# Kernel optimization log

Hardware: AMD Instinct MI355X
Metric: run time of the kernel (lower is better)

## Reference

```python
import jax, jax.numpy as jnp
import numpy as np

MAX_LENGTH = 400
NULL_TERM_IND = 52
THR = 1.0 - 1e-05  # F.threshold threshold value


def leaky(x):
    # F.leaky_relu default negative_slope=0.01
    return jnp.where(x >= 0, x, 0.01 * x)


def gru_cell(x, h, w_ih, w_hh, b_ih, b_hh):
    # torch.nn.GRUCell math
    gi = x @ w_ih.T + b_ih          # [B, 3H]
    gh = h @ w_hh.T + b_hh          # [B, 3H]
    i_r, i_z, i_n = jnp.split(gi, 3, axis=-1)
    h_r, h_z, h_n = jnp.split(gh, 3, axis=-1)
    r = jax.nn.sigmoid(i_r + h_r)
    z = jax.nn.sigmoid(i_z + h_z)
    n = jnp.tanh(i_n + r * h_n)
    return (1.0 - z) * n + z * h


def setup_inputs() -> dict:
    key = jax.random.key(0)
    ks = jax.random.split(key, 9)
    B, D, H, C = 2048, 4096, 128, 96
    def init(k, shape, fan):
        return (jax.random.uniform(k, shape, jnp.float32) * 2.0 - 1.0) / np.sqrt(fan)
    return {
        "img_feat": jax.random.normal(ks[0], (B, D), jnp.float32),
        "lin1_w": init(ks[1], (H, D), D),
        "lin1_b": init(ks[2], (H,), D),
        "w_ih": init(ks[3], (3 * H, H), H),
        "w_hh": init(ks[4], (3 * H, H), H),
        "b_ih": init(ks[5], (3 * H,), H),
        "b_hh": init(ks[6], (3 * H,), H),
        "lin2_w": init(ks[7], (C, H), H),
        "lin2_b": init(ks[8], (C,), H),
    }


def reference(img_feat, lin1_w, lin1_b, w_ih, w_hh, b_ih, b_hh, lin2_w, lin2_b):
    # ht: GRU input at t=0 is leaky_relu(lin1(img_feat)); hidden starts at zeros.
    ht = leaky(img_feat @ lin1_w.T + lin1_b)   # [B, 128]
    h0 = jnp.zeros_like(ht)

    def step(carry, _):
        ht, h0 = carry
        hn = gru_cell(ht, h0, w_ih, w_hh, b_ih, b_hh)
        # original: ht = char_gen(ht, h0); h0 = ht -> input == hidden next step
        chars = leaky(hn) @ lin2_w.T + lin2_b   # [B, C]
        m = jax.lax.stop_gradient(jnp.max(chars, axis=-1, keepdims=True))  # .data detach
        cn = chars / m
        cn = jnp.where(cn > THR, cn, 0.0)       # F.threshold(x, 1-1e-5, 0)
        return (hn, hn), cn

    _, titles = jax.lax.scan(step, (ht, h0), None, length=MAX_LENGTH)  # [T, B, C]
    titles = jnp.transpose(titles, (1, 0, 2))   # [B, T, C]

    # title_lens: first t with titles[b, t, NULL_TERM_IND] == 1, else MAX_LENGTH
    eq = titles[:, :, NULL_TERM_IND] == 1.0     # [B, T]
    first = jnp.argmax(eq, axis=1)
    lens = jnp.where(eq.any(axis=1), first + 1, MAX_LENGTH).astype(jnp.int32)
    return titles, lens
```

## Files before the change

kernel.cpp:

```cpp
#include <hip/hip_runtime.h>
#include <math.h>

#define NB   8
#define TT   400
#define HH   128
#define CC   96
#define DD   4096
#define THRV (1.0f - 1e-5f)
#define XR   40
#define HEPS 4e-6f
#define CHP  128
#define S10  1024.0f
#define IS10 0.0009765625f
#define IS20 9.5367431640625e-07f

typedef _Float16 f16x8 __attribute__((ext_vector_type(8)));
typedef float    f32x4 __attribute__((ext_vector_type(4)));

__device__ __forceinline__ float rcp_fast(float x) {
#if __has_builtin(__builtin_amdgcn_rcpf)
    return __builtin_amdgcn_rcpf(x);
#else
    return 1.0f / x;
#endif
}
__device__ __forceinline__ float sigm(float v)  { return rcp_fast(1.0f + __expf(-v)); }
__device__ __forceinline__ float ftanh(float x) { return 1.0f - 2.0f * rcp_fast(1.0f + __expf(2.0f * x)); }

__device__ __forceinline__ void split2(float4 u0, float4 u1, f16x8& hi, f16x8& lo) {
    float x[8] = {u0.x, u0.y, u0.z, u0.w, u1.x, u1.y, u1.z, u1.w};
    #pragma unroll
    for (int e = 0; e < 8; ++e) {
        _Float16 h = (_Float16)x[e];
        hi[e] = h;
        lo[e] = (_Float16)(x[e] - (float)h);
    }
}
__device__ __forceinline__ void split2s(float4 u0, float4 u1, f16x8& hi, f16x8& lo) {
    float x[8] = {u0.x, u0.y, u0.z, u0.w, u1.x, u1.y, u1.z, u1.w};
    #pragma unroll
    for (int e = 0; e < 8; ++e) {
        _Float16 h = (_Float16)x[e];
        hi[e] = h;
        lo[e] = (_Float16)((x[e] - (float)h) * S10);
    }
}
__device__ __forceinline__ void split1(float x, _Float16& hi, _Float16& lo) {
    hi = (_Float16)x;
    lo = (_Float16)(x - (float)hi);
}

__device__ __forceinline__ float xsum32(float v) {
#if __has_builtin(__builtin_amdgcn_permlane32_swap)
    auto r = __builtin_amdgcn_permlane32_swap(__float_as_uint(v), __float_as_uint(v), false, false);
    return __uint_as_float(r[0]) + __uint_as_float(r[1]);
#else
    return v + __shfl_xor(v, 32, 64);
#endif
}

__device__ __forceinline__ void step_barrier() {
    __builtin_amdgcn_sched_barrier(0);
    asm volatile("s_waitcnt lgkmcnt(0)" ::: "memory");
    __builtin_amdgcn_s_barrier();
    asm volatile("" ::: "memory");
    __builtin_amdgcn_sched_barrier(0);
}

__global__ __launch_bounds__(512)
void gru_title(const float* __restrict__ img,
               const float* __restrict__ l1w,
               const float* __restrict__ l1b,
               const float* __restrict__ wih,
               const float* __restrict__ whh,
               const float* __restrict__ bih,
               const float* __restrict__ bhh,
               const float* __restrict__ l2w,
               const float* __restrict__ l2b,
               float* __restrict__ out,
               float* __restrict__ lens)
{
    __shared__ alignas(16) _Float16 x2 [2][64][XR];
    __shared__ alignas(16) _Float16 l2v[2][64][XR];
    __shared__ alignas(16) float    chs[2][NB][CHP];
    __shared__ alignas(16) _Float16 bclS[6][4][4][16][8];
    __shared__ alignas(16) float    gsT[4][HH][NB];
    __shared__ alignas(16) float    xs0[NB][HH];
    __shared__ int sh_st[4];

    const int tid  = threadIdx.x;
    const int b0   = blockIdx.x * NB;
    const int w    = tid >> 6;
    const int lane = tid & 63;
    const int lm   = lane & 15;
    const int lq   = lane >> 4;

    f16x8 bh[4][4], bl[4][4];
    float gb[4];
    const int ic = 16 * w + lm;
    #pragma unroll
    for (int g = 0; g < 4; ++g) {
        const float* r0;
        const float* r1 = nullptr;
        float bsum;
        if (g == 0)      { r0 = wih + (size_t)ic * HH;         r1 = whh + (size_t)ic * HH;         bsum = bih[ic] + bhh[ic]; }
        else if (g == 1) { r0 = wih + (size_t)(128 + ic) * HH; r1 = whh + (size_t)(128 + ic) * HH; bsum = bih[128 + ic] + bhh[128 + ic]; }
        else if (g == 2) { r0 = wih + (size_t)(256 + ic) * HH;                                     bsum = bih[256 + ic]; }
        else             { r0 = whh + (size_t)(256 + ic) * HH;                                     bsum = bhh[256 + ic]; }
        gb[g] = bsum;
        #pragma unroll
        for (int kt = 0; kt < 4; ++kt) {
            const int k0 = 32 * kt + 8 * lq;
            float4 u0 = *(const float4*)(r0 + k0);
            float4 u1 = *(const float4*)(r0 + k0 + 4);
            if (r1) {
                float4 e0 = *(const float4*)(r1 + k0);
                float4 e1 = *(const float4*)(r1 + k0 + 4);
                u0.x += e0.x; u0.y += e0.y; u0.z += e0.z; u0.w += e0.w;
                u1.x += e1.x; u1.y += e1.y; u1.z += e1.z; u1.w += e1.w;
            }
            split2(u0, u1, bh[g][kt], bl[g][kt]);
        }
    }

    const int cw = (w == 1) ? 0 : (w == 3) ? 1 : (w == 6) ? 2 : -1;
    f16x8 bch[2][4];
    float cb[2] = {0.f, 0.f};
    if (cw >= 0) {
        #pragma unroll
        for (int u = 0; u < 2; ++u) {
            const int n = 16 * (2 * cw + u) + lm;
            cb[u] = l2b[n];
            #pragma unroll
            for (int kt = 0; kt < 4; ++kt) {
                const int k0 = 32 * kt + 8 * lq;
                float4 u0 = *(const float4*)(l2w + (size_t)n * HH + k0);
                float4 u1 = *(const float4*)(l2w + (size_t)n * HH + k0 + 4);
                f16x8 hi, lo;
                split2(u0, u1, hi, lo);
                bch[u][kt] = hi;
            }
        }
    }
    for (int idx = tid; idx < 6 * 4 * 4 * 16; idx += 512) {
        int t_  = idx;
        int lm_ = t_ & 15; t_ >>= 4;
        int lq_ = t_ & 3;  t_ >>= 2;
        int kt_ = t_ & 3;  t_ >>= 2;
        int ct_ = t_;
        const int n  = 16 * ct_ + lm_;
        const int k0 = 32 * kt_ + 8 * lq_;
        #pragma unroll
        for (int e = 0; e < 8; ++e) {
            float v = l2w[(size_t)n * HH + k0 + e];
            _Float16 hi = (_Float16)v;
            bclS[ct_][kt_][lq_][lm_][e] = (_Float16)(v - (float)hi);
        }
    }

    if (tid < 4) sh_st[tid] = 1;

    {
        const int m8 = lm & 7;
        const float* arow = img + (size_t)(b0 + m8) * DD + 8 * lq;
        const float* brow = l1w + (size_t)(16 * w + lm) * DD + 8 * lq;
        f32x4 z4 = {0.f, 0.f, 0.f, 0.f};
        f32x4 accP0 = z4, accP1 = z4, accQ0 = z4, accQ1 = z4;
        auto ptile = [&](int kt, f32x4& aP, f32x4& aQ) {
            float4 a0  = *(const float4*)(arow + 32 * kt);
            float4 a1  = *(const float4*)(arow + 32 * kt + 4);
            float4 bb0 = *(const float4*)(brow + 32 * kt);
            float4 bb1 = *(const float4*)(brow + 32 * kt + 4);
            f16x8 ah, al, bhf, blf;
            split2s(a0, a1, ah, al);
            split2s(bb0, bb1, bhf, blf);
            f16x8 af = (lm >= 8) ? al : ah;
            aP = __builtin_amdgcn_mfma_f32_16x16x32_f16(af, bhf, aP, 0, 0, 0);
            aQ = __builtin_amdgcn_mfma_f32_16x16x32_f16(af, blf, aQ, 0, 0, 0);
        };
        #pragma unroll 2
        for (int kt = 0; kt < DD / 32; kt += 2) {
            ptile(kt,     accP0, accQ0);
            ptile(kt + 1, accP1, accQ1);
        }
        f32x4 P = accP0 + accP1;
        f32x4 Q = accQ0 + accQ1;
        const float sP = (lane < 32) ? 1.0f  : IS10;
        const float sQ = (lane < 32) ? IS10 : IS20;
        float s0 = xsum32(P[0] * sP + Q[0] * sQ);
        float s1 = xsum32(P[1] * sP + Q[1] * sQ);
        float s2 = xsum32(P[2] * sP + Q[2] * sQ);
        float s3 = xsum32(P[3] * sP + Q[3] * sQ);
        if (lane < 32) {
            const int c = 16 * w + lm;
            const float bb = l1b[c];
            float vv[4] = {s0, s1, s2, s3};
            #pragma unroll
            for (int reg = 0; reg < 4; ++reg) {
                float h0 = vv[reg] + bb;
                xs0[4 * lq + reg][c] = (h0 >= 0.f) ? h0 : 0.01f * h0;
            }
        }
    }
    __syncthreads();

    const int mA  = (lane < 32) ? 4 * lq : 4 * (lq - 2) + 2;
    const int iN  = ic;
    const int rB_ = 16 * ((iN >> 3) & 3);
    const int cB_ = 8 * (iN >> 5) + (iN & 7);

    float hA = 0.f, hB = 0.f;
    int  len   = TT;
    bool found = false;
    int  tex   = TT;

    auto chars_mfma = [&](int slot, f32x4& c0, f32x4& c1) {
        #pragma unroll
        for (int kt = 0; kt < 4; ++kt) {
            f16x8 cf  = *(const f16x8*)&l2v[slot][lane][8 * kt];
            f16x8 wl0 = *(const f16x8*)&bclS[2 * cw + 0][kt][lq][lm][0];
            f16x8 wl1 = *(const f16x8*)&bclS[2 * cw + 1][kt][lq][lm][0];
            c0 = __builtin_amdgcn_mfma_f32_16x16x32_f16(cf, bch[0][kt], c0, 0, 0, 0);
            c0 = __builtin_amdgcn_mfma_f32_16x16x32_f16(cf, wl0,        c0, 0, 0, 0);
            c1 = __builtin_amdgcn_mfma_f32_16x16x32_f16(cf, bch[1][kt], c1, 0, 0, 0);
            c1 = __builtin_amdgcn_mfma_f32_16x16x32_f16(cf, wl1,        c1, 0, 0, 0);
        }
    };
    auto chars_commit = [&](int slot, f32x4 c0, f32x4 c1) {
        #pragma unroll
        for (int u = 0; u < 2; ++u) {
            f32x4 ca = u ? c1 : c0;
            const int n = 16 * (2 * cw + u) + lm;
            float s0 = xsum32(ca[0]);
            float s1 = xsum32(ca[1]);
            float s2 = xsum32(ca[2]);
            float s3 = xsum32(ca[3]);
            chs[slot][mA][n]     = ((lane < 32) ? s0 : s2) + cb[u];
            chs[slot][mA + 1][n] = ((lane < 32) ? s1 : s3) + cb[u];
        }
    };

    auto outrow = [&](int slot, int tme) {
        const float* cr = &chs[slot][w][0];
        float a0 = cr[lane];
        float a1 = cr[32 + lane];
        float a2 = cr[64 + lane];
        float mx = fmaxf(fmaxf(a0, a1), a2);
        mx = fmaxf(mx, __shfl_xor(mx, 16, 32));
        mx = fmaxf(mx, __shfl_xor(mx, 8, 32));
        mx = fmaxf(mx, __shfl_xor(mx, 4, 32));
        mx = fmaxf(mx, __shfl_xor(mx, 2, 32));
        mx = fmaxf(mx, __shfl_xor(mx, 1, 32));
        float q0 = a0 / mx;
        float q1 = a1 / mx;
        float q2 = a2 / mx;
        if (lane < 32) {
            size_t base = ((size_t)(b0 + w) * TT + tme) * CC;
            out[base + lane]      = (q0 > THRV) ? q0 : 0.f;
            out[base + 32 + lane] = (q1 > THRV) ? q1 : 0.f;
            out[base + 64 + lane] = (q2 > THRV) ? q2 : 0.f;
        }
        float q52 = __shfl(q1, 20, 64);
        if (!found && q52 == 1.0f) { found = true; len = tme + 1; }
    };

    for (int t = 0; t < TT; ++t) {
        const int pr = (t + 1) & 1;
        const int pc = t & 1;

        float G[4][2];

        if (t == 0) {
            {
                const int g = tid >> 7;
                const int i = tid & 127;
                float bsum;
                if (g == 0)      bsum = bih[i] + bhh[i];
                else if (g == 1) bsum = bih[128 + i] + bhh[128 + i];
                else if (g == 2) bsum = bih[256 + i];
                else             bsum = bhh[256 + i];
                float accT[NB];
                #pragma unroll
                for (int m = 0; m < NB; ++m) accT[m] = bsum;
                if (g < 3) {
                    const float4* wp = (const float4*)(wih + (size_t)(128 * g + i) * HH);
                    #pragma unroll
                    for (int k = 0; k < HH / 4; ++k) {
                        float4 wv = wp[k];
                        #pragma unroll
                        for (int m = 0; m < NB; ++m) {
                            float4 x = *(const float4*)&xs0[m][4 * k];
                            accT[m] += wv.x * x.x + wv.y * x.y + wv.z * x.z + wv.w * x.w;
                        }
                    }
                }
                float4 lo4 = {accT[0], accT[1], accT[2], accT[3]};
                float4 hi4 = {accT[4], accT[5], accT[6], accT[7]};
                *(float4*)&gsT[g][i][0] = lo4;
                *(float4*)&gsT[g][i][4] = hi4;
            }
            step_barrier();
            #pragma unroll
            for (int g = 0; g < 4; ++g) {
                float2 p = *(const float2*)&gsT[g][iN][mA];
                G[g][0] = p.x;
                G[g][1] = p.y;
            }
        } else {
            f16x8 af0 = *(const f16x8*)&x2[pr][lane][0];
            f16x8 af1 = *(const f16x8*)&x2[pr][lane][8];
            f16x8 af2 = *(const f16x8*)&x2[pr][lane][16];
            f16x8 af3 = *(const f16x8*)&x2[pr][lane][24];
            f32x4 z4 = {0.f, 0.f, 0.f, 0.f};
            f32x4 aA[4] = {z4, z4, z4, z4};
            f32x4 aB[4] = {z4, z4, z4, z4};
            #pragma unroll
            for (int g = 0; g < 4; ++g) {
                aA[g] = __builtin_amdgcn_mfma_f32_16x16x32_f16(af0, bh[g][0], aA[g], 0, 0, 0);
                aA[g] = __builtin_amdgcn_mfma_f32_16x16x32_f16(af0, bl[g][0], aA[g], 0, 0, 0);
                aA[g] = __builtin_amdgcn_mfma_f32_16x16x32_f16(af1, bh[g][1], aA[g], 0, 0, 0);
                aA[g] = __builtin_amdgcn_mfma_f32_16x16x32_f16(af1, bl[g][1], aA[g], 0, 0, 0);
                aB[g] = __builtin_amdgcn_mfma_f32_16x16x32_f16(af2, bh[g][2], aB[g], 0, 0, 0);
                aB[g] = __builtin_amdgcn_mfma_f32_16x16x32_f16(af2, bl[g][2], aB[g], 0, 0, 0);
                aB[g] = __builtin_amdgcn_mfma_f32_16x16x32_f16(af3, bh[g][3], aB[g], 0, 0, 0);
                aB[g] = __builtin_amdgcn_mfma_f32_16x16x32_f16(af3, bl[g][3], aB[g], 0, 0, 0);
            }
            f32x4 cc0 = z4, cc1 = z4;
            if (cw >= 0) chars_mfma(pr, cc0, cc1);
            if (t >= 2) outrow(pc, t - 2);
            #pragma unroll
            for (int g = 0; g < 4; ++g) {
                f32x4 s4 = aA[g] + aB[g];
                float s0 = xsum32(s4[0]);
                float s1 = xsum32(s4[1]);
                float s2 = xsum32(s4[2]);
                float s3 = xsum32(s4[3]);
                G[g][0] = ((lane < 32) ? s0 : s2) + gb[g];
                G[g][1] = ((lane < 32) ? s1 : s3) + gb[g];
            }
            if (cw >= 0) chars_commit(pr, cc0, cc1);
        }

        bool chg = (t < 2);
        #pragma unroll
        for (int s = 0; s < 2; ++s) {
            float hp = s ? hB : hA;
            float r  = sigm(G[0][s]);
            float z  = sigm(G[1][s]);
            float n  = ftanh(G[2][s] + r * G[3][s]);
            float h  = (1.f - z) * n + z * hp;
            chg |= (fabsf(h - hp) > HEPS);
            float lv = (h >= 0.f) ? h : 0.01f * h;
            _Float16 a, b;
            split1(h, a, b);
            x2[pc][rB_ + mA + s][cB_]     = a;
            x2[pc][rB_ + 8 + mA + s][cB_] = b;
            split1(lv, a, b);
            l2v[pc][rB_ + mA + s][cB_]     = a;
            l2v[pc][rB_ + 8 + mA + s][cB_] = b;
            if (s) hB = h; else hA = h;
        }
        if (chg) sh_st[t & 3] = 0;
        if (tid == 0) sh_st[(t + 2) & 3] = 1;
        step_barrier();
        if (t >= 2 && sh_st[t & 3]) { tex = t; break; }
    }

    if (tex == TT) {
        const int pl = (TT - 1) & 1;
        if (cw >= 0) {
            f32x4 z4 = {0.f, 0.f, 0.f, 0.f};
            f32x4 cc0 = z4, cc1 = z4;
            chars_mfma(pl, cc0, cc1);
            chars_commit(pl, cc0, cc1);
        }
        outrow(TT & 1, TT - 2);
        __syncthreads();
        outrow(pl, TT - 1);
    } else {
        outrow((tex + 1) & 1, tex - 1);
        size_t rowbase = (size_t)(b0 + w) * TT * CC;
        #pragma unroll
        for (int p = 0; p < 2; ++p) {
            const float* cr = &chs[p][w][0];
            float a0 = cr[lane];
            float a1 = cr[32 + lane];
            float a2 = cr[64 + lane];
            float mx = fmaxf(fmaxf(a0, a1), a2);
            mx = fmaxf(mx, __shfl_xor(mx, 16, 32));
            mx = fmaxf(mx, __shfl_xor(mx, 8, 32));
            mx = fmaxf(mx, __shfl_xor(mx, 4, 32));
            mx = fmaxf(mx, __shfl_xor(mx, 2, 32));
            mx = fmaxf(mx, __shfl_xor(mx, 1, 32));
            const int u0 = tex + (((tex & 1) == p) ? 0 : 1);
            if (lane < 32) {
                float q0 = a0 / mx;
                float q1 = a1 / mx;
                float q2 = a2 / mx;
                float w0v = (q0 > THRV) ? q0 : 0.f;
                float w1v = (q1 > THRV) ? q1 : 0.f;
                float w2v = (q2 > THRV) ? q2 : 0.f;
                for (int u = u0; u < TT; u += 2) {
                    out[rowbase + (size_t)u * CC + lane]      = w0v;
                    out[rowbase + (size_t)u * CC + 32 + lane] = w1v;
                    out[rowbase + (size_t)u * CC + 64 + lane] = w2v;
                }
            }
        }
    }

    if (lane == 0) lens[b0 + w] = (float)len;
}

extern "C" void kernel_launch(void* const* d_in, const int* in_sizes, int n_in,
                              void* d_out, int out_size, void* d_ws, size_t ws_size,
                              hipStream_t stream)
{
    const float* img = (const float*)d_in[0];
    const float* l1w = (const float*)d_in[1];
    const float* l1b = (const float*)d_in[2];
    const float* wih = (const float*)d_in[3];
    const float* whh = (const float*)d_in[4];
    const float* bih = (const float*)d_in[5];
    const float* bhh = (const float*)d_in[6];
    const float* l2w = (const float*)d_in[7];
    const float* l2b = (const float*)d_in[8];

    float* out  = (float*)d_out;
    float* lens = out + (size_t)2048 * TT * CC;

    gru_title<<<dim3(2048 / NB), dim3(512), 0, stream>>>(
        img, l1w, l1b, wih, whh, bih, bhh, l2w, l2b, out, lens);
}
```

Baseline: 651.7 us.

## Double block to 1024 threads, split GRU gates across waves via LDS exchange

```diff
diff --git a/kernel.cpp b/kernel.cpp
--- a/kernel.cpp
+++ b/kernel.cpp
@@ -9,13 +9,13 @@
 #define THRV (1.0f - 1e-5f)
 #define XR   40
 #define HEPS 4e-6f
-#define CHP  128
 #define S10  1024.0f
 #define IS10 0.0009765625f
 #define IS20 9.5367431640625e-07f
 
 typedef _Float16 f16x8 __attribute__((ext_vector_type(8)));
 typedef float    f32x4 __attribute__((ext_vector_type(4)));
+typedef float    f32x2 __attribute__((ext_vector_type(2)));
 
 __device__ __forceinline__ float rcp_fast(float x) {
 #if __has_builtin(__builtin_amdgcn_rcpf)
@@ -67,7 +67,7 @@
     __builtin_amdgcn_sched_barrier(0);
 }
 
-__global__ __launch_bounds__(512)
+__global__ __launch_bounds__(1024)
 void gru_title(const float* __restrict__ img,
                const float* __restrict__ l1w,
                const float* __restrict__ l1b,
@@ -82,9 +82,9 @@
 {
     __shared__ alignas(16) _Float16 x2 [2][64][XR];
     __shared__ alignas(16) _Float16 l2v[2][64][XR];
-    __shared__ alignas(16) float    chs[2][NB][CHP];
-    __shared__ alignas(16) _Float16 bclS[6][4][4][16][8];
-    __shared__ alignas(16) float    gsT[4][HH][NB];
+    __shared__ alignas(16) _Float16 bcS[2][6][4][4][16][8];
+    __shared__ alignas(16) float    gEx[4096];
+    __shared__ alignas(16) float    scr[2048];
     __shared__ alignas(16) float    xs0[NB][HH];
     __shared__ int sh_st[4];
 
@@ -94,20 +94,23 @@
     const int lane = tid & 63;
     const int lm   = lane & 15;
     const int lq   = lane >> 4;
-
-    f16x8 bh[4][4], bl[4][4];
-    float gb[4];
-    const int ic = 16 * w + lm;
+    const int c8   = w & 7;
+    const int r8   = w >> 3;
+    const int ic2  = 16 * c8 + lm;
+
+    f16x8 bh[2][4], bl[2][4];
+    float gb[2];
     #pragma unroll
-    for (int g = 0; g < 4; ++g) {
+    for (int gl = 0; gl < 2; ++gl) {
+        const int g2 = 2 * r8 + gl;
         const float* r0;
         const float* r1 = nullptr;
         float bsum;
-        if (g == 0)      { r0 = wih + (size_t)ic * HH;         r1 = whh + (size_t)ic * HH;         bsum = bih[ic] + bhh[ic]; }
-        else if (g == 1) { r0 = wih + (size_t)(128 + ic) * HH; r1 = whh + (size_t)(128 + ic) * HH; bsum = bih[128 + ic] + bhh[128 + ic]; }
-        else if (g == 2) { r0 = wih + (size_t)(256 + ic) * HH;                                     bsum = bih[256 + ic]; }
-        else             { r0 = whh + (size_t)(256 + ic) * HH;                                     bsum = bhh[256 + ic]; }
-        gb[g] = bsum;
+        if (g2 == 0)      { r0 = wih + (size_t)ic2 * HH;         r1 = whh + (size_t)ic2 * HH;         bsum = bih[ic2] + bhh[ic2]; }
+        else if (g2 == 1) { r0 = wih + (size_t)(128 + ic2) * HH; r1 = whh + (size_t)(128 + ic2) * HH; bsum = bih[128 + ic2] + bhh[128 + ic2]; }
+        else if (g2 == 2) { r0 = wih + (size_t)(256 + ic2) * HH;                                      bsum = bih[256 + ic2]; }
+        else              { r0 = whh + (size_t)(256 + ic2) * HH;                                      bsum = bhh[256 + ic2]; }
+        gb[gl] = bsum;
         #pragma unroll
         for (int kt = 0; kt < 4; ++kt) {
             const int k0 = 32 * kt + 8 * lq;
@@ -119,30 +122,15 @@
                 u0.x += e0.x; u0.y += e0.y; u0.z += e0.z; u0.w += e0.w;
                 u1.x += e1.x; u1.y += e1.y; u1.z += e1.z; u1.w += e1.w;
             }
-            split2(u0, u1, bh[g][kt], bl[g][kt]);
-        }
-    }
-
-    const int cw = (w == 1) ? 0 : (w == 3) ? 1 : (w == 6) ? 2 : -1;
-    f16x8 bch[2][4];
-    float cb[2] = {0.f, 0.f};
-    if (cw >= 0) {
-        #pragma unroll
-        for (int u = 0; u < 2; ++u) {
-            const int n = 16 * (2 * cw + u) + lm;
-            cb[u] = l2b[n];
-            #pragma unroll
-            for (int kt = 0; kt < 4; ++kt) {
-                const int k0 = 32 * kt + 8 * lq;
-                float4 u0 = *(const float4*)(l2w + (size_t)n * HH + k0);
-                float4 u1 = *(const float4*)(l2w + (size_t)n * HH + k0 + 4);
-                f16x8 hi, lo;
-                split2(u0, u1, hi, lo);
-                bch[u][kt] = hi;
-            }
-        }
-    }
-    for (int idx = tid; idx < 6 * 4 * 4 * 16; idx += 512) {
+            split2(u0, u1, bh[gl][kt], bl[gl][kt]);
+        }
+    }
+
+    const int ct = (w >= 1 && w <= 6) ? (w - 1) : -1;
+    float cb = 0.f;
+    if (ct >= 0) cb = l2b[16 * ct + lm];
+
+    for (int idx = tid; idx < 6 * 4 * 4 * 16; idx += 1024) {
         int t_  = idx;
         int lm_ = t_ & 15; t_ >>= 4;
         int lq_ = t_ & 3;  t_ >>= 2;
@@ -154,7 +142,8 @@
         for (int e = 0; e < 8; ++e) {
             float v = l2w[(size_t)n * HH + k0 + e];
             _Float16 hi = (_Float16)v;
-            bclS[ct_][kt_][lq_][lm_][e] = (_Float16)(v - (float)hi);
+            bcS[0][ct_][kt_][lq_][lm_][e] = hi;
+            bcS[1][ct_][kt_][lq_][lm_][e] = (_Float16)(v - (float)hi);
         }
     }
 
@@ -162,8 +151,8 @@
 
     {
         const int m8 = lm & 7;
-        const float* arow = img + (size_t)(b0 + m8) * DD + 8 * lq;
-        const float* brow = l1w + (size_t)(16 * w + lm) * DD + 8 * lq;
+        const float* arow = img + (size_t)(b0 + m8) * DD + 8 * lq + 2048 * r8;
+        const float* brow = l1w + (size_t)ic2 * DD + 8 * lq + 2048 * r8;
         f32x4 z4 = {0.f, 0.f, 0.f, 0.f};
         f32x4 accP0 = z4, accP1 = z4, accQ0 = z4, accQ1 = z4;
         auto ptile = [&](int kt, f32x4& aP, f32x4& aQ) {
@@ -179,69 +168,70 @@
             aQ = __builtin_amdgcn_mfma_f32_16x16x32_f16(af, blf, aQ, 0, 0, 0);
         };
         #pragma unroll 2
-        for (int kt = 0; kt < DD / 32; kt += 2) {
+        for (int kt = 0; kt < 64; kt += 2) {
             ptile(kt,     accP0, accQ0);
             ptile(kt + 1, accP1, accQ1);
         }
         f32x4 P = accP0 + accP1;
         f32x4 Q = accQ0 + accQ1;
-        const float sP = (lane < 32) ? 1.0f  : IS10;
+        const float sP = (lane < 32) ? 1.0f : IS10;
         const float sQ = (lane < 32) ? IS10 : IS20;
         float s0 = xsum32(P[0] * sP + Q[0] * sQ);
         float s1 = xsum32(P[1] * sP + Q[1] * sQ);
         float s2 = xsum32(P[2] * sP + Q[2] * sQ);
         float s3 = xsum32(P[3] * sP + Q[3] * sQ);
         if (lane < 32) {
-            const int c = 16 * w + lm;
-            const float bb = l1b[c];
             float vv[4] = {s0, s1, s2, s3};
             #pragma unroll
-            for (int reg = 0; reg < 4; ++reg) {
-                float h0 = vv[reg] + bb;
-                xs0[4 * lq + reg][c] = (h0 >= 0.f) ? h0 : 0.01f * h0;
-            }
+            for (int reg = 0; reg < 4; ++reg)
+                scr[r8 * 1024 + (4 * lq + reg) * 128 + ic2] = vv[reg];
         }
     }
     __syncthreads();
-
-    const int mA  = (lane < 32) ? 4 * lq : 4 * (lq - 2) + 2;
-    const int iN  = ic;
-    const int rB_ = 16 * ((iN >> 3) & 3);
-    const int cB_ = 8 * (iN >> 5) + (iN & 7);
-
-    float hA = 0.f, hB = 0.f;
+    {
+        const int m = tid >> 7, c = tid & 127;
+        float v = scr[m * 128 + c] + scr[1024 + m * 128 + c] + l1b[c];
+        xs0[m][c] = (v >= 0.f) ? v : 0.01f * v;
+    }
+    __syncthreads();
+
+    const int mA = (lane < 32) ? 4 * lq : 4 * (lq - 2) + 2;
+
+    const int mB  = w >> 1;
+    const int iB  = 64 * (w & 1) + lane;
+    const int rBq = 16 * ((iB >> 3) & 3);
+    const int cBq = 8 * (iB >> 5) + (iB & 7);
+    const unsigned gRd = (unsigned)(mB * 2048 + iB * 16) ^ ((unsigned)(mB & 3) << 5);
+
+    float hreg = 0.f;
     int  len   = TT;
     bool found = false;
     int  tex   = TT;
 
-    auto chars_mfma = [&](int slot, f32x4& c0, f32x4& c1) {
+    auto chars_mfma = [&](int slot, f32x4& cA, f32x4& cB) {
         #pragma unroll
         for (int kt = 0; kt < 4; ++kt) {
-            f16x8 cf  = *(const f16x8*)&l2v[slot][lane][8 * kt];
-            f16x8 wl0 = *(const f16x8*)&bclS[2 * cw + 0][kt][lq][lm][0];
-            f16x8 wl1 = *(const f16x8*)&bclS[2 * cw + 1][kt][lq][lm][0];
-            c0 = __builtin_amdgcn_mfma_f32_16x16x32_f16(cf, bch[0][kt], c0, 0, 0, 0);
-            c0 = __builtin_amdgcn_mfma_f32_16x16x32_f16(cf, wl0,        c0, 0, 0, 0);
-            c1 = __builtin_amdgcn_mfma_f32_16x16x32_f16(cf, bch[1][kt], c1, 0, 0, 0);
-            c1 = __builtin_amdgcn_mfma_f32_16x16x32_f16(cf, wl1,        c1, 0, 0, 0);
+            f16x8 cf = *(const f16x8*)&l2v[slot][lane][8 * kt];
+            f16x8 bH = *(const f16x8*)&bcS[0][ct][kt][lq][lm][0];
+            f16x8 bL = *(const f16x8*)&bcS[1][ct][kt][lq][lm][0];
+            f32x4& a = (kt < 2) ? cA : cB;
+            a = __builtin_amdgcn_mfma_f32_16x16x32_f16(cf, bH, a, 0, 0, 0);
+            a = __builtin_amdgcn_mfma_f32_16x16x32_f16(cf, bL, a, 0, 0, 0);
         }
     };
-    auto chars_commit = [&](int slot, f32x4 c0, f32x4 c1) {
-        #pragma unroll
-        for (int u = 0; u < 2; ++u) {
-            f32x4 ca = u ? c1 : c0;
-            const int n = 16 * (2 * cw + u) + lm;
-            float s0 = xsum32(ca[0]);
-            float s1 = xsum32(ca[1]);
-            float s2 = xsum32(ca[2]);
-            float s3 = xsum32(ca[3]);
-            chs[slot][mA][n]     = ((lane < 32) ? s0 : s2) + cb[u];
-            chs[slot][mA + 1][n] = ((lane < 32) ? s1 : s3) + cb[u];
-        }
+    auto chars_commit = [&](int slot, f32x4 cA, f32x4 cB) {
+        f32x4 ca = cA + cB;
+        const int n = 16 * ct + lm;
+        float s0 = xsum32(ca[0]);
+        float s1 = xsum32(ca[1]);
+        float s2 = xsum32(ca[2]);
+        float s3 = xsum32(ca[3]);
+        scr[slot * 1024 + mA * 128 + n]       = ((lane < 32) ? s0 : s2) + cb;
+        scr[slot * 1024 + (mA + 1) * 128 + n] = ((lane < 32) ? s1 : s3) + cb;
     };
 
-    auto outrow = [&](int slot, int tme) {
-        const float* cr = &chs[slot][w][0];
+    auto outrow = [&](int slot, int tme, int r) {
+        const float* cr = &scr[slot * 1024 + r * 128];
         float a0 = cr[lane];
         float a1 = cr[32 + lane];
         float a2 = cr[64 + lane];
@@ -255,7 +245,7 @@
         float q1 = a1 / mx;
         float q2 = a2 / mx;
         if (lane < 32) {
-            size_t base = ((size_t)(b0 + w) * TT + tme) * CC;
+            size_t base = ((size_t)(b0 + r) * TT + tme) * CC;
             out[base + lane]      = (q0 > THRV) ? q0 : 0.f;
             out[base + 32 + lane] = (q1 > THRV) ? q1 : 0.f;
             out[base + 64 + lane] = (q2 > THRV) ? q2 : 0.f;
@@ -268,10 +258,8 @@
         const int pr = (t + 1) & 1;
         const int pc = t & 1;
 
-        float G[4][2];
-
         if (t == 0) {
-            {
+            if (tid < 512) {
                 const int g = tid >> 7;
                 const int i = tid & 127;
                 float bsum;
@@ -294,17 +282,11 @@
                         }
                     }
                 }
-                float4 lo4 = {accT[0], accT[1], accT[2], accT[3]};
-                float4 hi4 = {accT[4], accT[5], accT[6], accT[7]};
-                *(float4*)&gsT[g][i][0] = lo4;
-                *(float4*)&gsT[g][i][4] = hi4;
-            }
-            step_barrier();
-            #pragma unroll
-            for (int g = 0; g < 4; ++g) {
-                float2 p = *(const float2*)&gsT[g][iN][mA];
-                G[g][0] = p.x;
-                G[g][1] = p.y;
+                #pragma unroll
+                for (int m = 0; m < NB; ++m) {
+                    unsigned off = (unsigned)(m * 2048 + i * 16 + g * 4) ^ ((unsigned)(m & 3) << 5);
+                    *(float*)((char*)gEx + off) = accT[m];
+                }
             }
         } else {
             f16x8 af0 = *(const f16x8*)&x2[pr][lane][0];
@@ -312,55 +294,63 @@
             f16x8 af2 = *(const f16x8*)&x2[pr][lane][16];
             f16x8 af3 = *(const f16x8*)&x2[pr][lane][24];
             f32x4 z4 = {0.f, 0.f, 0.f, 0.f};
-            f32x4 aA[4] = {z4, z4, z4, z4};
-            f32x4 aB[4] = {z4, z4, z4, z4};
+            f32x4 aA[2] = {z4, z4};
+            f32x4 aB[2] = {z4, z4};
             #pragma unroll
-            for (int g = 0; g < 4; ++g) {
-                aA[g] = __builtin_amdgcn_mfma_f32_16x16x32_f16(af0, bh[g][0], aA[g], 0, 0, 0);
-                aA[g] = __builtin_amdgcn_mfma_f32_16x16x32_f16(af0, bl[g][0], aA[g], 0, 0, 0);
-                aA[g] = __builtin_amdgcn_mfma_f32_16x16x32_f16(af1, bh[g][1], aA[g], 0, 0, 0);
-                aA[g] = __builtin_amdgcn_mfma_f32_16x16x32_f16(af1, bl[g][1], aA[g], 0, 0, 0);
-                aB[g] = __builtin_amdgcn_mfma_f32_16x16x32_f16(af2, bh[g][2], aB[g], 0, 0, 0);
-                aB[g] = __builtin_amdgcn_mfma_f32_16x16x32_f16(af2, bl[g][2], aB[g], 0, 0, 0);
-                aB[g] = __builtin_amdgcn_mfma_f32_16x16x32_f16(af3, bh[g][3], aB[g], 0, 0, 0);
-                aB[g] = __builtin_amdgcn_mfma_f32_16x16x32_f16(af3, bl[g][3], aB[g], 0, 0, 0);
+            for (int gl = 0; gl < 2; ++gl) {
+                aA[gl] = __builtin_amdgcn_mfma_f32_16x16x32_f16(af0, bh[gl][0], aA[gl], 0, 0, 0);
+                aA[gl] = __builtin_amdgcn_mfma_f32_16x16x32_f16(af0, bl[gl][0], aA[gl], 0, 0, 0);
+                aA[gl] = __builtin_amdgcn_mfma_f32_16x16x32_f16(af1, bh[gl][1], aA[gl], 0, 0, 0);
+                aA[gl] = __builtin_amdgcn_mfma_f32_16x16x32_f16(af1, bl[gl][1], aA[gl], 0, 0, 0);
+                aB[gl] = __builtin_amdgcn_mfma_f32_16x16x32_f16(af2, bh[gl][2], aB[gl], 0, 0, 0);
+                aB[gl] = __builtin_amdgcn_mfma_f32_16x16x32_f16(af2, bl[gl][2], aB[gl], 0, 0, 0);
+                aB[gl] = __builtin_amdgcn_mfma_f32_16x16x32_f16(af3, bh[gl][3], aB[gl], 0, 0, 0);
+                aB[gl] = __builtin_amdgcn_mfma_f32_16x16x32_f16(af3, bl[gl][3], aB[gl], 0, 0, 0);
             }
             f32x4 cc0 = z4, cc1 = z4;
-            if (cw >= 0) chars_mfma(pr, cc0, cc1);
-            if (t >= 2) outrow(pc, t - 2);
+            if (ct >= 0) chars_mfma(pr, cc0, cc1);
+            float G[2][2];
             #pragma unroll
-            for (int g = 0; g < 4; ++g) {
-                f32x4 s4 = aA[g] + aB[g];
+            for (int gl = 0; gl < 2; ++gl) {
+                f32x4 s4 = aA[gl] + aB[gl];
                 float s0 = xsum32(s4[0]);
                 float s1 = xsum32(s4[1]);
                 float s2 = xsum32(s4[2]);
                 float s3 = xsum32(s4[3]);
-                G[g][0] = ((lane < 32) ? s0 : s2) + gb[g];
-                G[g][1] = ((lane < 32) ? s1 : s3) + gb[g];
-            }
-            if (cw >= 0) chars_commit(pr, cc0, cc1);
-        }
-
-        bool chg = (t < 2);
-        #pragma unroll
-        for (int s = 0; s < 2; ++s) {
-            float hp = s ? hB : hA;
-            float r  = sigm(G[0][s]);
-            float z  = sigm(G[1][s]);
-            float n  = ftanh(G[2][s] + r * G[3][s]);
+                G[gl][0] = ((lane < 32) ? s0 : s2) + gb[gl];
+                G[gl][1] = ((lane < 32) ? s1 : s3) + gb[gl];
+            }
+            #pragma unroll
+            for (int s = 0; s < 2; ++s) {
+                const int m = mA + s;
+                unsigned off = (unsigned)(m * 2048 + ic2 * 16 + r8 * 8) ^ ((unsigned)(m & 3) << 5);
+                f32x2 v2 = {G[0][s], G[1][s]};
+                *(f32x2*)((char*)gEx + off) = v2;
+            }
+            if (ct >= 0) chars_commit(pr, cc0, cc1);
+        }
+        step_barrier();
+
+        {
+            float4 g4 = *(const float4*)((const char*)gEx + gRd);
+            float r = sigm(g4.x);
+            float z = sigm(g4.y);
+            float n = ftanh(g4.z + r * g4.w);
+            float hp = (t == 0) ? 0.f : hreg;
             float h  = (1.f - z) * n + z * hp;
-            chg |= (fabsf(h - hp) > HEPS);
+            bool chg = (t < 2) | (fabsf(h - hp) > HEPS);
+            hreg = h;
             float lv = (h >= 0.f) ? h : 0.01f * h;
             _Float16 a, b;
             split1(h, a, b);
-            x2[pc][rB_ + mA + s][cB_]     = a;
-            x2[pc][rB_ + 8 + mA + s][cB_] = b;
+            x2[pc][rBq + mB][cBq]     = a;
+            x2[pc][rBq + 8 + mB][cBq] = b;
             split1(lv, a, b);
-            l2v[pc][rB_ + mA + s][cB_]     = a;
-            l2v[pc][rB_ + 8 + mA + s][cB_] = b;
-            if (s) hB = h; else hA = h;
-        }
-        if (chg) sh_st[t & 3] = 0;
+            l2v[pc][rBq + mB][cBq]     = a;
+            l2v[pc][rBq + 8 + mB][cBq] = b;
+            if (chg) sh_st[t & 3] = 0;
+        }
+        if (w >= 8 && t >= 2) outrow(pc, t - 2, w - 8);
         if (tid == 0) sh_st[(t + 2) & 3] = 1;
         step_barrier();
         if (t >= 2 && sh_st[t & 3]) { tex = t; break; }
@@ -368,21 +358,22 @@
 
     if (tex == TT) {
         const int pl = (TT - 1) & 1;
-        if (cw >= 0) {
+        if (ct >= 0) {
             f32x4 z4 = {0.f, 0.f, 0.f, 0.f};
             f32x4 cc0 = z4, cc1 = z4;
             chars_mfma(pl, cc0, cc1);
             chars_commit(pl, cc0, cc1);
         }
-        outrow(TT & 1, TT - 2);
+        if (w >= 8) outrow(TT & 1, TT - 2, w - 8);
         __syncthreads();
-        outrow(pl, TT - 1);
-    } else {
-        outrow((tex + 1) & 1, tex - 1);
-        size_t rowbase = (size_t)(b0 + w) * TT * CC;
+        if (w >= 8) outrow(pl, TT - 1, w - 8);
+    } else if (w >= 8) {
+        const int r = w - 8;
+        outrow((tex + 1) & 1, tex - 1, r);
+        size_t rowbase = (size_t)(b0 + r) * TT * CC;
         #pragma unroll
         for (int p = 0; p < 2; ++p) {
-            const float* cr = &chs[p][w][0];
+            const float* cr = &scr[p * 1024 + r * 128];
             float a0 = cr[lane];
             float a1 = cr[32 + lane];
             float a2 = cr[64 + lane];
@@ -409,7 +400,7 @@
         }
     }
 
-    if (lane == 0) lens[b0 + w] = (float)len;
+    if (w >= 8 && lane == 0) lens[b0 + (w - 8)] = (float)len;
 }
 
 extern "C" void kernel_launch(void* const* d_in, const int* in_sizes, int n_in,
@@ -429,6 +420,6 @@
     float* out  = (float*)d_out;
     float* lens = out + (size_t)2048 * TT * CC;
 
-    gru_title<<<dim3(2048 / NB), dim3(512), 0, stream>>>(
+    gru_title<<<dim3(2048 / NB), dim3(1024), 0, stream>>>(
         img, l1w, l1b, wih, whh, bih, bhh, l2w, l2b, out, lens);
 }
```

Result: faster. 633.6 us (-2.8%).
